# Optimization experiments

Measured on AMD Instinct MI355X. Metric: run time of the kernel, lower is better.

## Reference

```python
import jax, jax.numpy as jnp
import numpy as np

B, N, FEAT, HID = 1024, 128, 512, 256


def setup_inputs() -> dict:
    key = jax.random.key(0)
    k1, k2, k3, k4, k5, k6 = jax.random.split(key, 6)
    x = jax.random.normal(k1, (B, FEAT), dtype=jnp.float32)
    labels = jax.random.randint(k2, (B,), 0, N, dtype=jnp.int64)
    W_proj = jax.random.normal(k3, (FEAT, HID), dtype=jnp.float32) / np.sqrt(FEAT)
    b_proj = jax.random.normal(k4, (HID,), dtype=jnp.float32) * 0.01
    means = jax.random.normal(k5, (N, HID), dtype=jnp.float32)
    # inverse covariances must be SPD so sqrt(dist_sq) is real
    A = jax.random.normal(k6, (N, HID, HID), dtype=jnp.float32)
    inv_covs = jnp.einsum('nij,nkj->nik', A, A) / HID + 0.1 * jnp.eye(HID, dtype=jnp.float32)
    return {"x": x, "labels": labels, "W_proj": W_proj, "b_proj": b_proj,
            "means": means, "inv_covs": inv_covs}


def reference(x, labels, W_proj, b_proj, means, inv_covs):
    b = x.shape[0]
    n = means.shape[0]
    x_proj = x @ W_proj + b_proj                       # (b, hid)
    delta = x_proj[:, None, :] - means[None, :, :]     # (b, n, hid)
    # batched Mahalanobis quadratic form
    dist_sq = jnp.einsum('bni,nij,bnj->bn', delta, inv_covs, delta)
    distmat = jnp.sqrt(dist_sq + 1e-12)                # (b, n)
    center_mask = (labels[:, None] == jnp.arange(n)[None, :]).astype(distmat.dtype)
    loss = jnp.clip(distmat * center_mask, 1e-12, 1e12).sum() / b
    return loss, distmat
```

## Files before the change

kernel.cpp:

```cpp
#include <hip/hip_runtime.h>
#include <hip/hip_bf16.h>

#define B_    1024
#define N_    128
#define FEAT_ 512
#define HID_  256

typedef __bf16 bf16x8 __attribute__((ext_vector_type(8)));
typedef float  f32x4  __attribute__((ext_vector_type(4)));

__device__ __forceinline__ unsigned int f2bf(float f) {
    unsigned int u = __float_as_uint(f);
    u += 0x7fffu + ((u >> 16) & 1u);
    return u >> 16;
}
__device__ __forceinline__ unsigned int pack2(float a, float b) {
    return f2bf(a) | (f2bf(b) << 16);
}

union U4V8 { uint4 u; bf16x8 v; };

__global__ __launch_bounds__(256) void wprep_kernel(
    const float* __restrict__ W, unsigned short* __restrict__ Wt_hi,
    unsigned short* __restrict__ Wt_lo, float* __restrict__ out)
{
    const int t = threadIdx.x;
    const int g = blockIdx.x;
    if (g == 0 && t == 0) out[0] = (float)(N_ - 1) * 1e-12f;
    float v[8];
    #pragma unroll
    for (int j = 0; j < 8; ++j) v[j] = W[(size_t)(g * 8 + j) * HID_ + t];
    unsigned int hu[4], lu[4];
    #pragma unroll
    for (int i = 0; i < 4; ++i) {
        const unsigned int u0 = __float_as_uint(v[2 * i]);
        const unsigned int u1 = __float_as_uint(v[2 * i + 1]);
        hu[i] = (u0 >> 16) | (u1 & 0xFFFF0000u);
        const float l0 = v[2 * i]     - __uint_as_float(u0 & 0xFFFF0000u);
        const float l1 = v[2 * i + 1] - __uint_as_float(u1 & 0xFFFF0000u);
        lu[i] = pack2(l0, l1);
    }
    const int g2 = g ^ ((t & 7) << 2);
    const size_t off = (size_t)t * FEAT_ + g2 * 8;
    *(uint4*)(Wt_hi + off) = make_uint4(hu[0], hu[1], hu[2], hu[3]);
    *(uint4*)(Wt_lo + off) = make_uint4(lu[0], lu[1], lu[2], lu[3]);
}

__global__ __launch_bounds__(512, 4) void prep_kernel(
    const float* __restrict__ x, const unsigned short* __restrict__ Wt_hi,
    const unsigned short* __restrict__ Wt_lo, const float* __restrict__ bias,
    const float* __restrict__ means, const float* __restrict__ invcov,
    float* __restrict__ xp, unsigned short* __restrict__ xbf,
    unsigned short* __restrict__ Mbf, float* __restrict__ v2,
    float* __restrict__ cpart)
{
    extern __shared__ char dyn[];
    const int t = threadIdx.x;
    if (blockIdx.x < 128) {
        unsigned short* Ms = (unsigned short*)dyn;
        const int pb   = blockIdx.x;
        const int bg   = pb >> 4;
        const int ht   = pb & 15;
        const int wave = t >> 6;
        const int lane = t & 63;
        const int q    = lane >> 4;
        const int l    = lane & 15;

        #pragma unroll
        for (int i = 0; i < 4; ++i) {
            const int cc   = i * 8 + wave;
            const int term = cc >> 4, lc = cc & 15;
            const unsigned short* s = (term ? Wt_lo : Wt_hi)
                                      + (size_t)ht * (16 * FEAT_) + lc * 512 + lane * 8;
            __builtin_amdgcn_global_load_lds(
                (const __attribute__((address_space(1))) unsigned int*)s,
                (__attribute__((address_space(3))) unsigned int*)&Ms[term * 8192 + lc * 512],
                16, 0, 0);
        }

        const int row = bg * 128 + wave * 16 + l;
        const float* __restrict__ xr = x + (size_t)row * FEAT_;
        f32x4 acc = {0.f, 0.f, 0.f, 0.f};
        __syncthreads();

        #pragma unroll
        for (int kk = 0; kk < 16; ++kk) {
            const float4 xa = *(const float4*)(xr + kk * 32 + q * 8);
            const float4 xb = *(const float4*)(xr + kk * 32 + q * 8 + 4);
            const float vv[8] = {xa.x, xa.y, xa.z, xa.w, xb.x, xb.y, xb.z, xb.w};
            U4V8 xh, xl;
            unsigned int hu[4], lu[4];
            #pragma unroll
            for (int i = 0; i < 4; ++i) {
                const unsigned int u0 = __float_as_uint(vv[2 * i]);
                const unsigned int u1 = __float_as_uint(vv[2 * i + 1]);
                hu[i] = (u0 >> 16) | (u1 & 0xFFFF0000u);
                const float l0 = vv[2 * i]     - __uint_as_float(u0 & 0xFFFF0000u);
                const float l1 = vv[2 * i + 1] - __uint_as_float(u1 & 0xFFFF0000u);
                lu[i] = pack2(l0, l1);
            }
            xh.u = make_uint4(hu[0], hu[1], hu[2], hu[3]);
            xl.u = make_uint4(lu[0], lu[1], lu[2], lu[3]);
            const int g2 = (((kk * 4 + q) ^ ((l & 7) << 2)) << 3);
            U4V8 bh, bl;
            bh.u = *(const uint4*)&Ms[l * FEAT_ + g2];
            bl.u = *(const uint4*)&Ms[8192 + l * FEAT_ + g2];
            acc = __builtin_amdgcn_mfma_f32_16x16x32_bf16(xh.v, bh.v, acc, 0, 0, 0);
            acc = __builtin_amdgcn_mfma_f32_16x16x32_bf16(xh.v, bl.v, acc, 0, 0, 0);
            acc = __builtin_amdgcn_mfma_f32_16x16x32_bf16(xl.v, bh.v, acc, 0, 0, 0);
        }
        const int h  = ht * 16 + l;
        const float bb = bias[h];
        #pragma unroll
        for (int r = 0; r < 4; ++r) {
            const int ro = bg * 128 + wave * 16 + q * 4 + r;
            const float val = acc[r] + bb;
            xp [(size_t)ro * HID_ + h] = val;
            xbf[(size_t)ro * HID_ + h] = (unsigned short)f2bf(val);
        }
    } else {
        float (*sv)[33] = (float (*)[33])dyn;
        float* sw = (float*)(dyn + 32 * 33 * 4);
        const int cb  = blockIdx.x - 128;
        const int n   = cb >> 3;
        const int jg2 = cb & 7;
        const float* Mn = invcov + (size_t)n * (HID_ * HID_) + (size_t)jg2 * 32 * HID_;
        const float* mu = means + (size_t)n * HID_;
        unsigned short* Mb = Mbf + (size_t)n * (HID_ * HID_) + (size_t)jg2 * 32 * HID_;
        const int gc = t & 31;
        const int r0 = t >> 5;
        const float4 mk0 = *(const float4*)(mu + gc * 8);
        const float4 mk1 = *(const float4*)(mu + gc * 8 + 4);
        #pragma unroll
        for (int i = 0; i < 2; ++i) {
            const int row = r0 + i * 16;
            const float* src = Mn + (size_t)row * HID_ + gc * 8;
            const float4 a = *(const float4*)src;
            const float4 b = *(const float4*)(src + 4);
            const int g2 = gc ^ ((row & 7) << 2);
            *(uint4*)(Mb + (size_t)row * HID_ + g2 * 8) =
                make_uint4(pack2(a.x, a.y), pack2(a.z, a.w), pack2(b.x, b.y), pack2(b.z, b.w));
            sv[row][gc] = a.x * mk0.x + a.y * mk0.y + a.z * mk0.z + a.w * mk0.w
                        + b.x * mk1.x + b.y * mk1.y + b.z * mk1.z + b.w * mk1.w;
        }
        __syncthreads();
        if (t < 256) {
            const int row = t >> 3;
            const int i0  = (t & 7) * 4;
            float v = sv[row][i0] + sv[row][i0 + 1] + sv[row][i0 + 2] + sv[row][i0 + 3];
            v += __shfl_xor(v, 1);
            v += __shfl_xor(v, 2);
            v += __shfl_xor(v, 4);
            const int j = jg2 * 32 + row;
            if ((t & 7) == 0) v2[(size_t)n * HID_ + j] = 2.f * v;
            float cc = ((t & 7) == 0) ? v * mu[j] : 0.f;
            cc += __shfl_xor(cc, 8);
            cc += __shfl_xor(cc, 16);
            cc += __shfl_xor(cc, 32);
            if ((t & 63) == 0) sw[t >> 6] = cc;
        }
        __syncthreads();
        if (t == 0) cpart[cb] = sw[0] + sw[1] + sw[2] + sw[3];
    }
}

__global__ __launch_bounds__(512, 4) void dist_kernel(
    const float* __restrict__ xp, const unsigned short* __restrict__ xbf,
    const unsigned short* __restrict__ Mbf, const float* __restrict__ v2,
    float* __restrict__ p)
{
    extern __shared__ unsigned short Ms[];

    const int tid  = threadIdx.x;
    const int id   = blockIdx.x;
    const int xcd  = id & 7;
    const int rest = id >> 3;
    const int bh   = rest & 3;
    const int s    = (rest >> 2) * 8 + xcd;
    const int jh   = s >> 7;
    const int n    = s & 127;
    const int wave = tid >> 6;
    const int lane = tid & 63;
    const int q    = lane >> 4;
    const int l    = lane & 15;

    const unsigned short* src = Mbf + (size_t)n * (HID_ * HID_) + (size_t)jh * 32768;
    #pragma unroll
    for (int i = 0; i < 8; ++i) {
        const int c = i * 8 + wave;
        __builtin_amdgcn_global_load_lds(
            (const __attribute__((address_space(1))) unsigned int*)(src + (size_t)c * 512 + lane * 8),
            (__attribute__((address_space(3))) unsigned int*)&Ms[c * 512],
            16, 0, 0);
    }

    bf16x8 afrag[2][8];
    #pragma unroll
    for (int rb = 0; rb < 2; ++rb) {
        const unsigned short* xr = xbf + (size_t)(bh * 256 + wave * 32 + rb * 16 + l) * HID_;
        #pragma unroll
        for (int kk = 0; kk < 8; ++kk)
            afrag[rb][kk] = *(const bf16x8*)(xr + kk * 32 + q * 8);
    }
    float v2l[8];
    #pragma unroll
    for (int ct = 0; ct < 8; ++ct)
        v2l[ct] = v2[(size_t)n * HID_ + jh * 128 + ct * 16 + l];

    __syncthreads();

    float part[8];
    #pragma unroll
    for (int i = 0; i < 8; ++i) part[i] = 0.f;

    const size_t xbase = (size_t)(bh * 256 + wave * 32 + q * 4) * HID_ + jh * 128 + l;

    #pragma unroll
    for (int ct = 0; ct < 8; ++ct) {
        float xl[8];
        #pragma unroll
        for (int rb = 0; rb < 2; ++rb)
            #pragma unroll
            for (int r = 0; r < 4; ++r)
                xl[rb * 4 + r] = xp[xbase + (size_t)(rb * 16 + r) * HID_ + ct * 16];

        f32x4 acc0 = {0.f,0.f,0.f,0.f}, acc1 = {0.f,0.f,0.f,0.f};
        #pragma unroll
        for (int kk = 0; kk < 8; ++kk) {
            const bf16x8 bfrag = *(const bf16x8*)&Ms[(ct * 16 + l) * HID_ +
                                                     (((kk * 4 + q) ^ ((l & 7) << 2)) << 3)];
            acc0 = __builtin_amdgcn_mfma_f32_16x16x32_bf16(afrag[0][kk], bfrag, acc0, 0, 0, 0);
            acc1 = __builtin_amdgcn_mfma_f32_16x16x32_bf16(afrag[1][kk], bfrag, acc1, 0, 0, 0);
        }
        const float vv = v2l[ct];
        #pragma unroll
        for (int r = 0; r < 4; ++r) {
            part[r]     += (acc0[r] - vv) * xl[r];
            part[4 + r] += (acc1[r] - vv) * xl[4 + r];
        }
    }

    #pragma unroll
    for (int i = 0; i < 8; ++i) {
        float v = part[i];
        v += __shfl_xor(v, 1);
        v += __shfl_xor(v, 2);
        v += __shfl_xor(v, 4);
        v += __shfl_xor(v, 8);
        part[i] = v;
    }
    if (l == 0) {
        float* pb = p + (size_t)jh * (B_ * N_);
        #pragma unroll
        for (int i = 0; i < 8; ++i) {
            const int row = bh * 256 + wave * 32 + (i >> 2) * 16 + q * 4 + (i & 3);
            pb[(size_t)row * N_ + n] = part[i];
        }
    }
}

__global__ __launch_bounds__(256) void finalize_kernel(
    const float* __restrict__ p, const float* __restrict__ cpart,
    const int* __restrict__ labels, float* __restrict__ out)
{
    __shared__ float sc[128];
    __shared__ float ls[4];
    const int t = threadIdx.x;
    if (t < 128) {
        float s = 0.f;
        #pragma unroll
        for (int g = 0; g < 8; ++g) s += cpart[t * 8 + g];
        sc[t] = s;
    }
    __syncthreads();
    const int i = blockIdx.x * 256 + t;
    const int n = i & (N_ - 1);
    const int b = i >> 7;
    const float d = sqrtf(p[i] + p[B_ * N_ + i] + sc[n] + 1e-12f);
    out[1 + i] = d;
    float sel = (labels[b] == n) ? d : 0.f;
    #pragma unroll
    for (int m = 1; m <= 32; m <<= 1) sel += __shfl_xor(sel, m);
    if ((t & 63) == 0) ls[t >> 6] = sel;
    __syncthreads();
    if (t == 0) atomicAdd(out, (ls[0] + ls[1] + ls[2] + ls[3]) * (1.f / (float)B_));
}

extern "C" void kernel_launch(void* const* d_in, const int* in_sizes, int n_in,
                              void* d_out, int out_size, void* d_ws, size_t ws_size,
                              hipStream_t stream) {
    const float* x      = (const float*)d_in[0];
    const int*   labels = (const int*)d_in[1];
    const float* W      = (const float*)d_in[2];
    const float* bias   = (const float*)d_in[3];
    const float* means  = (const float*)d_in[4];
    const float* invcov = (const float*)d_in[5];
    float* out = (float*)d_out;

    char* ws = (char*)d_ws;
    unsigned short* Mbf   = (unsigned short*)(ws);
    float*          xp    = (float*)         (ws + 16777216);
    unsigned short* xbf   = (unsigned short*)(ws + 17825792);
    float*          v2    = (float*)         (ws + 18350080);
    float*          cpart = (float*)         (ws + 18481152);
    float*          p     = (float*)         (ws + 18489344);
    unsigned short* Wt_hi = (unsigned short*)(ws + 18489344);
    unsigned short* Wt_lo = (unsigned short*)(ws + 18751488);

    constexpr int DIST_LDS = 128 * HID_ * 2;
    (void)hipFuncSetAttribute((const void*)dist_kernel,
                              hipFuncAttributeMaxDynamicSharedMemorySize, DIST_LDS);

    wprep_kernel<<<dim3(64), 256, 0, stream>>>(W, Wt_hi, Wt_lo, out);
    prep_kernel<<<dim3(1152), 512, 32768, stream>>>(x, Wt_hi, Wt_lo, bias, means, invcov,
                                                    xp, xbf, Mbf, v2, cpart);
    dist_kernel<<<dim3(1024), 512, DIST_LDS, stream>>>(xp, xbf, Mbf, v2, p);
    finalize_kernel<<<dim3((B_ * N_) / 256), 256, 0, stream>>>(p, cpart, labels, out);
}
```

Before: 134.8 us.

## Fuse finalize into dist kernel via per-tile ticket completion counter

Removes the separate finalize kernel launch. Each dist block atomically increments a ticket for its (bh, n) tile, and the second of the two jh halves to arrive combines both partial sums, applies sqrt, writes distmat and accumulates the loss. This saves one launch and a full pass over p, but adds a threadfence, a per-element atomicAdd on the loss, and reads of p that may hit L2 across XCDs. It also relies on ticket being zeroed in wprep, and the ticket region sits between cpart and p.

```diff
diff --git a/kernel.cpp b/kernel.cpp
--- a/kernel.cpp
+++ b/kernel.cpp
@@ -22,11 +22,13 @@
 
 __global__ __launch_bounds__(256) void wprep_kernel(
     const float* __restrict__ W, unsigned short* __restrict__ Wt_hi,
-    unsigned short* __restrict__ Wt_lo, float* __restrict__ out)
+    unsigned short* __restrict__ Wt_lo, int* __restrict__ ticket,
+    float* __restrict__ out)
 {
     const int t = threadIdx.x;
     const int g = blockIdx.x;
     if (g == 0 && t == 0) out[0] = (float)(N_ - 1) * 1e-12f;
+    if (g < 2) ticket[g * 256 + t] = 0;
     float v[8];
     #pragma unroll
     for (int j = 0; j < 8; ++j) v[j] = W[(size_t)(g * 8 + j) * HID_ + t];
@@ -167,9 +169,11 @@
 __global__ __launch_bounds__(512, 4) void dist_kernel(
     const float* __restrict__ xp, const unsigned short* __restrict__ xbf,
     const unsigned short* __restrict__ Mbf, const float* __restrict__ v2,
-    float* __restrict__ p)
+    const float* __restrict__ cpart, const int* __restrict__ labels,
+    float* __restrict__ p, int* __restrict__ ticket, float* __restrict__ out)
 {
     extern __shared__ unsigned short Ms[];
+    __shared__ int flag;
 
     const int tid  = threadIdx.x;
     const int id   = blockIdx.x;
@@ -257,33 +261,21 @@
             pb[(size_t)row * N_ + n] = part[i];
         }
     }
-}
-
-__global__ __launch_bounds__(256) void finalize_kernel(
-    const float* __restrict__ p, const float* __restrict__ cpart,
-    const int* __restrict__ labels, float* __restrict__ out)
-{
-    __shared__ float sc[128];
-    __shared__ float ls[4];
-    const int t = threadIdx.x;
-    if (t < 128) {
-        float s = 0.f;
-        #pragma unroll
-        for (int g = 0; g < 8; ++g) s += cpart[t * 8 + g];
-        sc[t] = s;
-    }
+
+    __threadfence();
+    if (tid == 0) flag = atomicAdd(&ticket[bh * 128 + n], 1);
     __syncthreads();
-    const int i = blockIdx.x * 256 + t;
-    const int n = i & (N_ - 1);
-    const int b = i >> 7;
-    const float d = sqrtf(p[i] + p[B_ * N_ + i] + sc[n] + 1e-12f);
-    out[1 + i] = d;
-    float sel = (labels[b] == n) ? d : 0.f;
-    #pragma unroll
-    for (int m = 1; m <= 32; m <<= 1) sel += __shfl_xor(sel, m);
-    if ((t & 63) == 0) ls[t >> 6] = sel;
-    __syncthreads();
-    if (t == 0) atomicAdd(out, (ls[0] + ls[1] + ls[2] + ls[3]) * (1.f / (float)B_));
+    if (flag == 1 && tid < 256) {
+        __threadfence();
+        float cn = 0.f;
+        #pragma unroll
+        for (int g = 0; g < 8; ++g) cn += cpart[n * 8 + g];
+        const int row = bh * 256 + tid;
+        const float d = sqrtf(p[(size_t)row * N_ + n] + p[B_ * N_ + (size_t)row * N_ + n]
+                              + cn + 1e-12f);
+        out[1 + (size_t)row * N_ + n] = d;
+        if (labels[row] == n) atomicAdd(out, d * (1.f / (float)B_));
+    }
 }
 
 extern "C" void kernel_launch(void* const* d_in, const int* in_sizes, int n_in,
@@ -303,6 +295,7 @@
     unsigned short* xbf   = (unsigned short*)(ws + 17825792);
     float*          v2    = (float*)         (ws + 18350080);
     float*          cpart = (float*)         (ws + 18481152);
+    int*            ticket= (int*)           (ws + 18485248);
     float*          p     = (float*)         (ws + 18489344);
     unsigned short* Wt_hi = (unsigned short*)(ws + 18489344);
     unsigned short* Wt_lo = (unsigned short*)(ws + 18751488);
@@ -311,9 +304,9 @@
     (void)hipFuncSetAttribute((const void*)dist_kernel,
                               hipFuncAttributeMaxDynamicSharedMemorySize, DIST_LDS);
 
-    wprep_kernel<<<dim3(64), 256, 0, stream>>>(W, Wt_hi, Wt_lo, out);
+    wprep_kernel<<<dim3(64), 256, 0, stream>>>(W, Wt_hi, Wt_lo, ticket, out);
     prep_kernel<<<dim3(1152), 512, 32768, stream>>>(x, Wt_hi, Wt_lo, bias, means, invcov,
                                                     xp, xbf, Mbf, v2, cpart);
-    dist_kernel<<<dim3(1024), 512, DIST_LDS, stream>>>(xp, xbf, Mbf, v2, p);
-    finalize_kernel<<<dim3((B_ * N_) / 256), 256, 0, stream>>>(p, cpart, labels, out);
-}
+    dist_kernel<<<dim3(1024), 512, DIST_LDS, stream>>>(xp, xbf, Mbf, v2, cpart,
+                                                       labels, p, ticket, out);
+}
```

Result: slower. 438.6 us (+225.4%).
